# Kernel optimization log

Measured on AMD Instinct MI355X. Metric: run time of the kernel, lower is better.

Reference implementation:

```python
import jax, jax.numpy as jnp
import numpy as np

B, L, F, H = 8, 1024, 1024, 16
D = F // H  # feat_head = 64
EPS = 1e-5


def setup_inputs() -> dict:
    key = jax.random.key(0)
    ks = jax.random.split(key, 12)
    s = 1.0 / np.sqrt(F)
    inp = {
        "q": jax.random.normal(ks[0], (B, L, F), jnp.float32),
        "k": jax.random.normal(ks[1], (B, L, F), jnp.float32),
        "v": jax.random.normal(ks[2], (B, L, F), jnp.float32),
        "Wq": jax.random.uniform(ks[3], (F, F), jnp.float32, -s, s),
        "bq": jax.random.uniform(ks[4], (F,), jnp.float32, -s, s),
        "Wk": jax.random.uniform(ks[5], (F, F), jnp.float32, -s, s),
        "bk": jax.random.uniform(ks[6], (F,), jnp.float32, -s, s),
        "Wv": jax.random.uniform(ks[7], (F, F), jnp.float32, -s, s),
        "bv": jax.random.uniform(ks[8], (F,), jnp.float32, -s, s),
        "Wf": jax.random.uniform(ks[9], (F, F), jnp.float32, -s, s),
        "bf": jax.random.uniform(ks[10], (F,), jnp.float32, -s, s),
        "gamma": jnp.ones((F,), jnp.float32),
        "beta": jnp.zeros((F,), jnp.float32),
    }
    return inp


def _split_heads(x):
    # (B, L, F) -> (B*H, L, D), matching reshape->transpose(1,2)->reshape
    return x.reshape(B, L, H, D).transpose(0, 2, 1, 3).reshape(B * H, L, D)


def reference(q, k, v, Wq, bq, Wk, bk, Wv, bv, Wf, bf, gamma, beta):
    residual = q
    qh = _split_heads(q @ Wq.T + bq)
    kh = _split_heads(k @ Wk.T + bk)
    vh = _split_heads(v @ Wv.T + bv)
    # scores: (B*H, L, L)
    scores = jnp.einsum('nqd,nkd->nqk', qh, kh) / np.sqrt(D)
    raw_att = jax.nn.softmax(scores, axis=-1)
    att = jnp.einsum('nqk,nkd->nqd', raw_att, vh)  # (B*H, L, D)
    # faithful to original output recombine: reshape(H, B, L, D).permute(1,2,0,3)
    att = att.reshape(H, B, L, D).transpose(1, 2, 0, 3).reshape(B, L, F)
    att = att @ Wf.T + bf
    # dropout in eval mode = identity; activation is None
    x = att + residual
    mu = jnp.mean(x, axis=-1, keepdims=True)
    var = jnp.mean(jnp.square(x - mu), axis=-1, keepdims=True)
    out = (x - mu) * jax.lax.rsqrt(var + EPS) * gamma + beta
    return out, raw_att
```

## Files before the change

### kernel.cpp

```cpp
#include <hip/hip_runtime.h>

#define BB 8
#define LL 1024
#define FF 1024
#define HH 16
#define DD 64
#define NBH 128

typedef __attribute__((ext_vector_type(8))) short bf16x8;
typedef __attribute__((ext_vector_type(4))) float f32x4;

#define GLD_LDS16(g, l)                                                        \
  __builtin_amdgcn_global_load_lds(                                            \
      (const __attribute__((address_space(1))) unsigned int*)(g),              \
      (__attribute__((address_space(3))) unsigned int*)(l), 16, 0, 0)

__device__ __forceinline__ unsigned short f2bf(float f) {
  unsigned int u = __float_as_uint(f);
  unsigned int r = u + 0x7fffu + ((u >> 16) & 1u);
  return (unsigned short)(r >> 16);
}

__global__ __launch_bounds__(256) void cvt3_kernel(const float* __restrict__ s0,
                                                   const float* __restrict__ s1,
                                                   const float* __restrict__ s2,
                                                   short* __restrict__ dst, int n4) {
  int z = blockIdx.y;
  const float* src = (z == 0) ? s0 : (z == 1) ? s1 : s2;
  int i = blockIdx.x * 256 + threadIdx.x;
  if (i >= n4) return;
  float4 v = ((const float4*)src)[i];
  short4 o;
  o.x = (short)f2bf(v.x); o.y = (short)f2bf(v.y);
  o.z = (short)f2bf(v.z); o.w = (short)f2bf(v.w);
  ((short4*)(dst + (size_t)z * n4 * 4))[i] = o;
}

__global__ __launch_bounds__(256) void cvt4_kernel(const float* __restrict__ s0,
                                                   const float* __restrict__ s1,
                                                   const float* __restrict__ s2,
                                                   const float* __restrict__ s3,
                                                   short* __restrict__ dst, int n4) {
  int z = blockIdx.y;
  const float* src = (z == 0) ? s0 : (z == 1) ? s1 : (z == 2) ? s2 : s3;
  int i = blockIdx.x * 256 + threadIdx.x;
  if (i >= n4) return;
  float4 v = ((const float4*)src)[i];
  short4 o;
  o.x = (short)f2bf(v.x); o.y = (short)f2bf(v.y);
  o.z = (short)f2bf(v.z); o.w = (short)f2bf(v.w);
  ((short4*)(dst + (size_t)z * n4 * 4))[i] = o;
}

__global__ __launch_bounds__(256) void proj_qkv(
    const short* __restrict__ Aall, const short* __restrict__ Wall,
    const float* __restrict__ bq, const float* __restrict__ bk,
    const float* __restrict__ bv, short* __restrict__ Dall) {
  const int o = blockIdx.x + (blockIdx.y << 6) + (blockIdx.z << 9);
  const int n = ((o & 7) * 192) + (o >> 3);
  const int z = n >> 9;
  const int r = n & 511;
  const int by = r & 7, bx = r >> 3;

  const short* A  = Aall + (size_t)z * (BB * LL * FF);
  const short* Bt = Wall + (size_t)z * (FF * FF);
  const float* bias = (z == 0) ? bq : (z == 1) ? bk : bv;
  short* dst = Dall + (size_t)z * ((size_t)NBH * LL * DD);
  const float scale = (z == 0) ? 0.125f : 1.0f;

  __shared__ __attribute__((aligned(16))) short As[128 * 64];
  __shared__ __attribute__((aligned(16))) short Bs[128 * 64];

  const int tid = threadIdx.x;
  const int lane = tid & 63, w = tid >> 6;
  const int wr = w >> 1, wc = w & 1;
  const int row16 = lane & 15, kg = lane >> 4;
  const int m0 = bx * 128, n0 = by * 128;

  const f32x4 z4 = {0.f, 0.f, 0.f, 0.f};
  f32x4 acc[4][4];
  for (int i = 0; i < 4; ++i)
    for (int j = 0; j < 4; ++j) acc[i][j] = z4;

  for (int k0 = 0; k0 < FF; k0 += 64) {
#pragma unroll
    for (int rr = 0; rr < 4; ++rr) {
      int e8 = tid + rr * 256;
      int row = e8 >> 3, cs = ((e8 & 7) ^ (row & 7)) * 8;
      GLD_LDS16(A + (size_t)(m0 + row) * FF + k0 + cs, As + e8 * 8);
      GLD_LDS16(Bt + (size_t)(n0 + row) * FF + k0 + cs, Bs + e8 * 8);
    }
    __syncthreads();
#pragma unroll
    for (int kk2 = 0; kk2 < 2; ++kk2) {
      bf16x8 af[4], bfr[4];
#pragma unroll
      for (int i = 0; i < 4; ++i) {
        int ra = wr * 64 + i * 16 + row16;
        int rb = wc * 64 + i * 16 + row16;
        af[i]  = *(const bf16x8*)(As + ra * 64 + ((((kk2 << 2) | kg) ^ (ra & 7)) << 3));
        bfr[i] = *(const bf16x8*)(Bs + rb * 64 + ((((kk2 << 2) | kg) ^ (rb & 7)) << 3));
      }
#pragma unroll
      for (int i = 0; i < 4; ++i)
#pragma unroll
        for (int j = 0; j < 4; ++j)
          acc[i][j] = __builtin_amdgcn_mfma_f32_16x16x32_bf16(af[i], bfr[j], acc[i][j], 0, 0, 0);
    }
    __syncthreads();
  }

#pragma unroll
  for (int i = 0; i < 4; ++i) {
#pragma unroll
    for (int j = 0; j < 4; ++j) {
      int ncol = n0 + wc * 64 + j * 16 + row16;
      float bn = bias[ncol];
      int h = ncol >> 6, d = ncol & 63;
#pragma unroll
      for (int rr = 0; rr < 4; ++rr) {
        int m = m0 + wr * 64 + i * 16 + kg * 4 + rr;
        int b = m >> 10, l = m & 1023;
        float val = (acc[i][j][rr] + bn) * scale;
        dst[(((size_t)(b * HH + h)) * LL + l) * DD + d] = (short)f2bf(val);
      }
    }
  }
}

__global__ __launch_bounds__(256) void vtrans(const short* __restrict__ Vh,
                                              short* __restrict__ Vt) {
  const int bh = blockIdx.y;
  const int l0 = blockIdx.x * 64;
  __shared__ short T[64][72];
  const int tid = threadIdx.x;
#pragma unroll
  for (int r = 0; r < 2; ++r) {
    int e = tid + r * 256;
    int row = e >> 3, c8 = (e & 7) * 8;
    *(uint4*)(&T[row][c8]) = *(const uint4*)(Vh + ((size_t)bh * LL + l0 + row) * DD + c8);
  }
  __syncthreads();
#pragma unroll
  for (int r = 0; r < 2; ++r) {
    int e = tid + r * 256;
    int d = e >> 3, l8 = (e & 7) * 8;
    short tmp[8];
#pragma unroll
    for (int j = 0; j < 8; ++j) tmp[j] = T[l8 + j][d];
    *(uint4*)(Vt + ((size_t)bh * DD + d) * LL + l0 + l8) = *(uint4*)tmp;
  }
}

__global__ __launch_bounds__(256) void attn_kernel(
    const short* __restrict__ Qh, const short* __restrict__ Kh,
    const short* __restrict__ Vt, float* __restrict__ Patt,
    short* __restrict__ attb) {
  const int o = blockIdx.x + (blockIdx.y << 4);
  const int n = ((o & 7) << 8) + (o >> 3);
  const int bh = n >> 4;
  const int q0 = (n & 15) * 64;
  const int tid = threadIdx.x;
  const int lane = tid & 63, w = tid >> 6;
  const int row16 = lane & 15, kg = lane >> 4;

  __shared__ __attribute__((aligned(16))) short Qs[64 * 64];
  __shared__ __attribute__((aligned(16))) short Ks[64 * 64];
  __shared__ __attribute__((aligned(16))) short Vts[64 * 64];
  __shared__ __attribute__((aligned(16))) short PsT[4][16 * 64];

#pragma unroll
  for (int r = 0; r < 2; ++r) {
    int e8 = tid + r * 256;
    int row = e8 >> 3, c8 = (e8 & 7) ^ (row & 7);
    GLD_LDS16(Qh + ((size_t)bh * LL + q0 + row) * DD + c8 * 8, Qs + e8 * 8);
  }
  __syncthreads();
  const int qrow = w * 16 + row16;
  bf16x8 aq0 = *(const bf16x8*)(Qs + qrow * 64 + ((kg ^ (qrow & 7)) << 3));
  bf16x8 aq1 = *(const bf16x8*)(Qs + qrow * 64 + (((kg + 4) ^ (qrow & 7)) << 3));

  const f32x4 z4 = {0.f, 0.f, 0.f, 0.f};
  float lsum = 0.f;

  for (int k0 = 0; k0 < LL; k0 += 64) {
#pragma unroll
    for (int r = 0; r < 2; ++r) {
      int e8 = tid + r * 256;
      int row = e8 >> 3, c8 = (e8 & 7) ^ (row & 7);
      GLD_LDS16(Kh + ((size_t)bh * LL + k0 + row) * DD + c8 * 8, Ks + e8 * 8);
    }
    __syncthreads();
    f32x4 s[4] = {z4, z4, z4, z4};
#pragma unroll
    for (int t = 0; t < 4; ++t) {
      int krow = t * 16 + row16;
      bf16x8 b0 = *(const bf16x8*)(Ks + krow * 64 + ((kg ^ (krow & 7)) << 3));
      bf16x8 b1 = *(const bf16x8*)(Ks + krow * 64 + (((kg + 4) ^ (krow & 7)) << 3));
      s[t] = __builtin_amdgcn_mfma_f32_16x16x32_bf16(b0, aq0, s[t], 0, 0, 0);
      s[t] = __builtin_amdgcn_mfma_f32_16x16x32_bf16(b1, aq1, s[t], 0, 0, 0);
    }
#pragma unroll
    for (int t = 0; t < 4; ++t)
#pragma unroll
      for (int r = 0; r < 4; ++r) lsum += __expf(s[t][r]);
    __syncthreads();
  }
  lsum += __shfl_xor(lsum, 16);
  lsum += __shfl_xor(lsum, 32);
  const float linv = 1.0f / lsum;

  f32x4 oT[4] = {z4, z4, z4, z4};

  for (int k0 = 0; k0 < LL; k0 += 64) {
#pragma unroll
    for (int r = 0; r < 2; ++r) {
      int e8 = tid + r * 256;
      int row = e8 >> 3, c8 = (e8 & 7) ^ (row & 7);
      GLD_LDS16(Kh + ((size_t)bh * LL + k0 + row) * DD + c8 * 8, Ks + e8 * 8);
      GLD_LDS16(Vt + ((size_t)bh * DD + row) * LL + k0 + c8 * 8, Vts + e8 * 8);
    }
    __syncthreads();
    f32x4 s[4] = {z4, z4, z4, z4};
#pragma unroll
    for (int t = 0; t < 4; ++t) {
      int krow = t * 16 + row16;
      bf16x8 b0 = *(const bf16x8*)(Ks + krow * 64 + ((kg ^ (krow & 7)) << 3));
      bf16x8 b1 = *(const bf16x8*)(Ks + krow * 64 + (((kg + 4) ^ (krow & 7)) << 3));
      s[t] = __builtin_amdgcn_mfma_f32_16x16x32_bf16(b0, aq0, s[t], 0, 0, 0);
      s[t] = __builtin_amdgcn_mfma_f32_16x16x32_bf16(b1, aq1, s[t], 0, 0, 0);
    }
    const int qq = q0 + w * 16 + row16;
#pragma unroll
    for (int t = 0; t < 4; ++t) {
      f32x4 pv;
#pragma unroll
      for (int r = 0; r < 4; ++r) pv[r] = __expf(s[t][r]) * linv;
      __builtin_nontemporal_store(
          pv, (f32x4*)(Patt + ((size_t)bh * LL + qq) * LL + k0 + t * 16 + kg * 4));
      short4 ps;
      ps.x = (short)f2bf(pv[0]); ps.y = (short)f2bf(pv[1]);
      ps.z = (short)f2bf(pv[2]); ps.w = (short)f2bf(pv[3]);
      int c = ((t * 2 + (kg >> 1)) ^ (row16 & 7));
      *(short4*)(&PsT[w][row16 * 64 + c * 8 + (kg & 1) * 4]) = ps;
    }
    bf16x8 pb0 = *(const bf16x8*)(&PsT[w][row16 * 64 + ((kg ^ (row16 & 7)) << 3)]);
    bf16x8 pb1 = *(const bf16x8*)(&PsT[w][row16 * 64 + (((4 + kg) ^ (row16 & 7)) << 3)]);
#pragma unroll
    for (int td = 0; td < 4; ++td) {
      int trow = td * 16 + row16;
      bf16x8 v0 = *(const bf16x8*)(Vts + trow * 64 + ((kg ^ (trow & 7)) << 3));
      bf16x8 v1 = *(const bf16x8*)(Vts + trow * 64 + (((kg + 4) ^ (trow & 7)) << 3));
      oT[td] = __builtin_amdgcn_mfma_f32_16x16x32_bf16(v0, pb0, oT[td], 0, 0, 0);
      oT[td] = __builtin_amdgcn_mfma_f32_16x16x32_bf16(v1, pb1, oT[td], 0, 0, 0);
    }
    __syncthreads();
  }

  const int iblk = bh >> 3;
  const int jb = bh & 7;
  const int qq = q0 + w * 16 + row16;
#pragma unroll
  for (int td = 0; td < 4; ++td) {
    short4 ov;
    ov.x = (short)f2bf(oT[td][0]); ov.y = (short)f2bf(oT[td][1]);
    ov.z = (short)f2bf(oT[td][2]); ov.w = (short)f2bf(oT[td][3]);
    *(short4*)(attb + ((size_t)jb * LL + qq) * FF + iblk * 64 + td * 16 + kg * 4) = ov;
  }
}

__global__ __launch_bounds__(256) void proj_out(
    const short* __restrict__ A, const short* __restrict__ Bt,
    const float* __restrict__ bias, const float* __restrict__ resid,
    float* __restrict__ xb) {
  const int o = blockIdx.x + (blockIdx.y << 6);
  const int n = ((o & 7) << 6) + (o >> 3);
  const int by = n & 7, bx = n >> 3;

  __shared__ __attribute__((aligned(16))) short As[128 * 64];
  __shared__ __attribute__((aligned(16))) short Bs[128 * 64];

  const int tid = threadIdx.x;
  const int lane = tid & 63, w = tid >> 6;
  const int wr = w >> 1, wc = w & 1;
  const int row16 = lane & 15, kg = lane >> 4;
  const int m0 = bx * 128, n0 = by * 128;

  const f32x4 z4 = {0.f, 0.f, 0.f, 0.f};
  f32x4 acc[4][4];
  for (int i = 0; i < 4; ++i)
    for (int j = 0; j < 4; ++j) acc[i][j] = z4;

  for (int k0 = 0; k0 < FF; k0 += 64) {
#pragma unroll
    for (int rr = 0; rr < 4; ++rr) {
      int e8 = tid + rr * 256;
      int row = e8 >> 3, cs = ((e8 & 7) ^ (row & 7)) * 8;
      GLD_LDS16(A + (size_t)(m0 + row) * FF + k0 + cs, As + e8 * 8);
      GLD_LDS16(Bt + (size_t)(n0 + row) * FF + k0 + cs, Bs + e8 * 8);
    }
    __syncthreads();
#pragma unroll
    for (int kk2 = 0; kk2 < 2; ++kk2) {
      bf16x8 af[4], bfr[4];
#pragma unroll
      for (int i = 0; i < 4; ++i) {
        int ra = wr * 64 + i * 16 + row16;
        int rb = wc * 64 + i * 16 + row16;
        af[i]  = *(const bf16x8*)(As + ra * 64 + ((((kk2 << 2) | kg) ^ (ra & 7)) << 3));
        bfr[i] = *(const bf16x8*)(Bs + rb * 64 + ((((kk2 << 2) | kg) ^ (rb & 7)) << 3));
      }
#pragma unroll
      for (int i = 0; i < 4; ++i)
#pragma unroll
        for (int j = 0; j < 4; ++j)
          acc[i][j] = __builtin_amdgcn_mfma_f32_16x16x32_bf16(af[i], bfr[j], acc[i][j], 0, 0, 0);
    }
    __syncthreads();
  }

#pragma unroll
  for (int i = 0; i < 4; ++i) {
#pragma unroll
    for (int j = 0; j < 4; ++j) {
      int ncol = n0 + wc * 64 + j * 16 + row16;
      float bn = bias[ncol];
#pragma unroll
      for (int rr = 0; rr < 4; ++rr) {
        int m = m0 + wr * 64 + i * 16 + kg * 4 + rr;
        xb[(size_t)m * FF + ncol] = acc[i][j][rr] + bn + resid[(size_t)m * FF + ncol];
      }
    }
  }
}

__global__ __launch_bounds__(256) void ln_kernel(const float* __restrict__ xb,
                                                 const float* __restrict__ gamma,
                                                 const float* __restrict__ beta,
                                                 float* __restrict__ out) {
  const int row = blockIdx.x;
  const int tid = threadIdx.x;
  const float4 v = *(const float4*)(xb + (size_t)row * FF + tid * 4);
  float s = v.x + v.y + v.z + v.w;
  float s2 = v.x * v.x + v.y * v.y + v.z * v.z + v.w * v.w;
#pragma unroll
  for (int o = 1; o < 64; o <<= 1) {
    s += __shfl_xor(s, o);
    s2 += __shfl_xor(s2, o);
  }
  __shared__ float ss[4], ss2[4];
  int w = tid >> 6, lane = tid & 63;
  if (lane == 0) { ss[w] = s; ss2[w] = s2; }
  __syncthreads();
  s = ss[0] + ss[1] + ss[2] + ss[3];
  s2 = ss2[0] + ss2[1] + ss2[2] + ss2[3];
  float mu = s * (1.0f / 1024.0f);
  float var = s2 * (1.0f / 1024.0f) - mu * mu;
  float rs = rsqrtf(var + 1e-5f);
  float4 g = *(const float4*)(gamma + tid * 4);
  float4 be = *(const float4*)(beta + tid * 4);
  float4 o;
  o.x = (v.x - mu) * rs * g.x + be.x;
  o.y = (v.y - mu) * rs * g.y + be.y;
  o.z = (v.z - mu) * rs * g.z + be.z;
  o.w = (v.w - mu) * rs * g.w + be.w;
  *(float4*)(out + (size_t)row * FF + tid * 4) = o;
}

extern "C" void kernel_launch(void* const* d_in, const int* in_sizes, int n_in,
                              void* d_out, int out_size, void* d_ws, size_t ws_size,
                              hipStream_t stream) {
  const float* q  = (const float*)d_in[0];
  const float* k  = (const float*)d_in[1];
  const float* v  = (const float*)d_in[2];
  const float* Wq = (const float*)d_in[3];
  const float* bq = (const float*)d_in[4];
  const float* Wk = (const float*)d_in[5];
  const float* bk = (const float*)d_in[6];
  const float* Wv = (const float*)d_in[7];
  const float* bv = (const float*)d_in[8];
  const float* Wf = (const float*)d_in[9];
  const float* bf = (const float*)d_in[10];
  const float* gamma = (const float*)d_in[11];
  const float* beta  = (const float*)d_in[12];

  float* out = (float*)d_out;
  float* Patt = out + (size_t)BB * LL * FF;

  char* ws = (char*)d_ws;
  const size_t MB = (size_t)1 << 20;
  short* qb = (short*)(ws + 0 * MB);
  short* Wb = (short*)(ws + 48 * MB);
  short* Qh = (short*)(ws + 56 * MB);
  short* Kh = (short*)(ws + 72 * MB);
  short* Vh = (short*)(ws + 88 * MB);
  short* attb = qb;
  short* Vt = (short*)(ws + 16 * MB);
  float* xb = (float*)(ws + 16 * MB);

  const int nAct4 = BB * LL * FF / 4;
  const int nW4 = FF * FF / 4;
  cvt3_kernel<<<dim3((nAct4 + 255) / 256, 3), 256, 0, stream>>>(q, k, v, qb, nAct4);
  cvt4_kernel<<<dim3((nW4 + 255) / 256, 4), 256, 0, stream>>>(Wq, Wk, Wv, Wf, Wb, nW4);

  proj_qkv<<<dim3(64, 8, 3), 256, 0, stream>>>(qb, Wb, bq, bk, bv, Qh);
  vtrans<<<dim3(16, 128), 256, 0, stream>>>(Vh, Vt);
  attn_kernel<<<dim3(16, 128), 256, 0, stream>>>(Qh, Kh, Vt, Patt, attb);
  proj_out<<<dim3(64, 8), 256, 0, stream>>>(attb, Wb + 3 * (size_t)FF * FF, bf, q, xb);
  ln_kernel<<<8192, 256, 0, stream>>>(xb, gamma, beta, out);
}
```

Baseline: 324.8 us.

## Fuse V transpose into QKV projection epilogue, double-buffer attention K/V tiles, use exp2

The QKV projection now stages its output tile in LDS and writes it back with coalesced 16-byte stores. For V it writes the tile transposed, which removes the separate vtrans kernel and its extra round trip through memory. The attention kernel double-buffers the K and V tiles so global-to-LDS loads overlap with MFMA work. It also folds log2(e) into the Q scale so softmax can use exp2 with a log-sum subtraction instead of exp followed by a multiply. The LDS footprint of proj_qkv grows and the attention kernel uses more shared memory, which may reduce occupancy.

```diff
diff --git a/kernel.cpp b/kernel.cpp
--- a/kernel.cpp
+++ b/kernel.cpp
@@ -66,10 +66,11 @@
   const short* Bt = Wall + (size_t)z * (FF * FF);
   const float* bias = (z == 0) ? bq : (z == 1) ? bk : bv;
   short* dst = Dall + (size_t)z * ((size_t)NBH * LL * DD);
-  const float scale = (z == 0) ? 0.125f : 1.0f;
-
-  __shared__ __attribute__((aligned(16))) short As[128 * 64];
-  __shared__ __attribute__((aligned(16))) short Bs[128 * 64];
+  const float scale = (z == 0) ? 0.125f * 1.44269504088896f : 1.0f;
+
+  __shared__ __attribute__((aligned(16))) short LB[128 * 136];
+  short* As = LB;
+  short* Bs = LB + 128 * 64;
 
   const int tid = threadIdx.x;
   const int lane = tid & 63, w = tid >> 6;
@@ -110,45 +111,39 @@
     __syncthreads();
   }
 
+  const int z2 = (z == 2);
 #pragma unroll
   for (int i = 0; i < 4; ++i) {
 #pragma unroll
     for (int j = 0; j < 4; ++j) {
-      int ncol = n0 + wc * 64 + j * 16 + row16;
-      float bn = bias[ncol];
-      int h = ncol >> 6, d = ncol & 63;
+      int nl = wc * 64 + j * 16 + row16;
+      float bn = bias[n0 + nl];
 #pragma unroll
       for (int rr = 0; rr < 4; ++rr) {
-        int m = m0 + wr * 64 + i * 16 + kg * 4 + rr;
-        int b = m >> 10, l = m & 1023;
+        int ml = wr * 64 + i * 16 + kg * 4 + rr;
         float val = (acc[i][j][rr] + bn) * scale;
-        dst[(((size_t)(b * HH + h)) * LL + l) * DD + d] = (short)f2bf(val);
+        int rrow = z2 ? nl : ml, ccol = z2 ? ml : nl;
+        LB[rrow * 136 + ccol] = (short)f2bf(val);
       }
     }
   }
-}
-
-__global__ __launch_bounds__(256) void vtrans(const short* __restrict__ Vh,
-                                              short* __restrict__ Vt) {
-  const int bh = blockIdx.y;
-  const int l0 = blockIdx.x * 64;
-  __shared__ short T[64][72];
-  const int tid = threadIdx.x;
-#pragma unroll
-  for (int r = 0; r < 2; ++r) {
-    int e = tid + r * 256;
-    int row = e >> 3, c8 = (e & 7) * 8;
-    *(uint4*)(&T[row][c8]) = *(const uint4*)(Vh + ((size_t)bh * LL + l0 + row) * DD + c8);
-  }
   __syncthreads();
-#pragma unroll
-  for (int r = 0; r < 2; ++r) {
-    int e = tid + r * 256;
-    int d = e >> 3, l8 = (e & 7) * 8;
-    short tmp[8];
-#pragma unroll
-    for (int j = 0; j < 8; ++j) tmp[j] = T[l8 + j][d];
-    *(uint4*)(Vt + ((size_t)bh * DD + d) * LL + l0 + l8) = *(uint4*)tmp;
+  const int b = m0 >> 10;
+  const int lbase = m0 & 1023;
+#pragma unroll
+  for (int rr = 0; rr < 8; ++rr) {
+    int e = tid + rr * 256;
+    int row = e >> 4, c8 = e & 15;
+    uint4 val = *(const uint4*)(LB + row * 136 + c8 * 8);
+    if (!z2) {
+      int l = lbase + row;
+      int h = (n0 + c8 * 8) >> 6, d = (c8 & 7) * 8;
+      *(uint4*)(dst + (((size_t)(b * HH + h)) * LL + l) * DD + d) = val;
+    } else {
+      int h = (n0 + row) >> 6, d = (n0 + row) & 63;
+      int l = lbase + c8 * 8;
+      *(uint4*)(dst + (((size_t)(b * HH + h)) * DD + d) * LL + l) = val;
+    }
   }
 }
 
@@ -165,16 +160,36 @@
   const int row16 = lane & 15, kg = lane >> 4;
 
   __shared__ __attribute__((aligned(16))) short Qs[64 * 64];
-  __shared__ __attribute__((aligned(16))) short Ks[64 * 64];
-  __shared__ __attribute__((aligned(16))) short Vts[64 * 64];
+  __shared__ __attribute__((aligned(16))) short Ks[2][64 * 64];
+  __shared__ __attribute__((aligned(16))) short Vts[2][64 * 64];
   __shared__ __attribute__((aligned(16))) short PsT[4][16 * 64];
 
-#pragma unroll
-  for (int r = 0; r < 2; ++r) {
-    int e8 = tid + r * 256;
-    int row = e8 >> 3, c8 = (e8 & 7) ^ (row & 7);
-    GLD_LDS16(Qh + ((size_t)bh * LL + q0 + row) * DD + c8 * 8, Qs + e8 * 8);
-  }
+#define STAGE_K(tt, bb)                                                        \
+  {                                                                            \
+    int e8a = tid, rowa = e8a >> 3, c8a = (e8a & 7) ^ (rowa & 7);              \
+    GLD_LDS16(Kh + ((size_t)bh * LL + (tt) * 64 + rowa) * DD + c8a * 8,        \
+              &Ks[bb][e8a * 8]);                                               \
+    int e8b = tid + 256, rowb = e8b >> 3, c8b = (e8b & 7) ^ (rowb & 7);        \
+    GLD_LDS16(Kh + ((size_t)bh * LL + (tt) * 64 + rowb) * DD + c8b * 8,        \
+              &Ks[bb][e8b * 8]);                                               \
+  }
+#define STAGE_V(tt, bb)                                                        \
+  {                                                                            \
+    int e8a = tid, rowa = e8a >> 3, c8a = (e8a & 7) ^ (rowa & 7);              \
+    GLD_LDS16(Vt + ((size_t)bh * DD + rowa) * LL + (tt) * 64 + c8a * 8,        \
+              &Vts[bb][e8a * 8]);                                              \
+    int e8b = tid + 256, rowb = e8b >> 3, c8b = (e8b & 7) ^ (rowb & 7);        \
+    GLD_LDS16(Vt + ((size_t)bh * DD + rowb) * LL + (tt) * 64 + c8b * 8,        \
+              &Vts[bb][e8b * 8]);                                              \
+  }
+
+  {
+    int e8a = tid, rowa = e8a >> 3, c8a = (e8a & 7) ^ (rowa & 7);
+    GLD_LDS16(Qh + ((size_t)bh * LL + q0 + rowa) * DD + c8a * 8, Qs + e8a * 8);
+    int e8b = tid + 256, rowb = e8b >> 3, c8b = (e8b & 7) ^ (rowb & 7);
+    GLD_LDS16(Qh + ((size_t)bh * LL + q0 + rowb) * DD + c8b * 8, Qs + e8b * 8);
+  }
+  STAGE_K(0, 0);
   __syncthreads();
   const int qrow = w * 16 + row16;
   bf16x8 aq0 = *(const bf16x8*)(Qs + qrow * 64 + ((kg ^ (qrow & 7)) << 3));
@@ -183,65 +198,61 @@
   const f32x4 z4 = {0.f, 0.f, 0.f, 0.f};
   float lsum = 0.f;
 
-  for (int k0 = 0; k0 < LL; k0 += 64) {
-#pragma unroll
-    for (int r = 0; r < 2; ++r) {
-      int e8 = tid + r * 256;
-      int row = e8 >> 3, c8 = (e8 & 7) ^ (row & 7);
-      GLD_LDS16(Kh + ((size_t)bh * LL + k0 + row) * DD + c8 * 8, Ks + e8 * 8);
-    }
-    __syncthreads();
+  for (int t = 0; t < 16; ++t) {
+    int cur = t & 1;
+    if (t < 15) STAGE_K(t + 1, cur ^ 1);
     f32x4 s[4] = {z4, z4, z4, z4};
 #pragma unroll
-    for (int t = 0; t < 4; ++t) {
-      int krow = t * 16 + row16;
-      bf16x8 b0 = *(const bf16x8*)(Ks + krow * 64 + ((kg ^ (krow & 7)) << 3));
-      bf16x8 b1 = *(const bf16x8*)(Ks + krow * 64 + (((kg + 4) ^ (krow & 7)) << 3));
-      s[t] = __builtin_amdgcn_mfma_f32_16x16x32_bf16(b0, aq0, s[t], 0, 0, 0);
-      s[t] = __builtin_amdgcn_mfma_f32_16x16x32_bf16(b1, aq1, s[t], 0, 0, 0);
-    }
-#pragma unroll
-    for (int t = 0; t < 4; ++t)
-#pragma unroll
-      for (int r = 0; r < 4; ++r) lsum += __expf(s[t][r]);
+    for (int tt = 0; tt < 4; ++tt) {
+      int krow = tt * 16 + row16;
+      bf16x8 b0 = *(const bf16x8*)(&Ks[cur][krow * 64 + ((kg ^ (krow & 7)) << 3)]);
+      bf16x8 b1 = *(const bf16x8*)(&Ks[cur][krow * 64 + (((kg + 4) ^ (krow & 7)) << 3)]);
+      s[tt] = __builtin_amdgcn_mfma_f32_16x16x32_bf16(b0, aq0, s[tt], 0, 0, 0);
+      s[tt] = __builtin_amdgcn_mfma_f32_16x16x32_bf16(b1, aq1, s[tt], 0, 0, 0);
+    }
+#pragma unroll
+    for (int tt = 0; tt < 4; ++tt)
+#pragma unroll
+      for (int rr = 0; rr < 4; ++rr) lsum += exp2f(s[tt][rr]);
     __syncthreads();
   }
   lsum += __shfl_xor(lsum, 16);
   lsum += __shfl_xor(lsum, 32);
-  const float linv = 1.0f / lsum;
+  const float lc = __log2f(lsum);
 
   f32x4 oT[4] = {z4, z4, z4, z4};
 
-  for (int k0 = 0; k0 < LL; k0 += 64) {
-#pragma unroll
-    for (int r = 0; r < 2; ++r) {
-      int e8 = tid + r * 256;
-      int row = e8 >> 3, c8 = (e8 & 7) ^ (row & 7);
-      GLD_LDS16(Kh + ((size_t)bh * LL + k0 + row) * DD + c8 * 8, Ks + e8 * 8);
-      GLD_LDS16(Vt + ((size_t)bh * DD + row) * LL + k0 + c8 * 8, Vts + e8 * 8);
-    }
-    __syncthreads();
+  STAGE_K(0, 0);
+  STAGE_V(0, 0);
+  __syncthreads();
+  for (int t = 0; t < 16; ++t) {
+    int cur = t & 1;
+    if (t < 15) {
+      STAGE_K(t + 1, cur ^ 1);
+      STAGE_V(t + 1, cur ^ 1);
+    }
     f32x4 s[4] = {z4, z4, z4, z4};
 #pragma unroll
-    for (int t = 0; t < 4; ++t) {
-      int krow = t * 16 + row16;
-      bf16x8 b0 = *(const bf16x8*)(Ks + krow * 64 + ((kg ^ (krow & 7)) << 3));
-      bf16x8 b1 = *(const bf16x8*)(Ks + krow * 64 + (((kg + 4) ^ (krow & 7)) << 3));
-      s[t] = __builtin_amdgcn_mfma_f32_16x16x32_bf16(b0, aq0, s[t], 0, 0, 0);
-      s[t] = __builtin_amdgcn_mfma_f32_16x16x32_bf16(b1, aq1, s[t], 0, 0, 0);
+    for (int tt = 0; tt < 4; ++tt) {
+      int krow = tt * 16 + row16;
+      bf16x8 b0 = *(const bf16x8*)(&Ks[cur][krow * 64 + ((kg ^ (krow & 7)) << 3)]);
+      bf16x8 b1 = *(const bf16x8*)(&Ks[cur][krow * 64 + (((kg + 4) ^ (krow & 7)) << 3)]);
+      s[tt] = __builtin_amdgcn_mfma_f32_16x16x32_bf16(b0, aq0, s[tt], 0, 0, 0);
+      s[tt] = __builtin_amdgcn_mfma_f32_16x16x32_bf16(b1, aq1, s[tt], 0, 0, 0);
     }
     const int qq = q0 + w * 16 + row16;
-#pragma unroll
-    for (int t = 0; t < 4; ++t) {
+    const int k0 = t * 64;
+#pragma unroll
+    for (int tt = 0; tt < 4; ++tt) {
       f32x4 pv;
 #pragma unroll
-      for (int r = 0; r < 4; ++r) pv[r] = __expf(s[t][r]) * linv;
+      for (int rr = 0; rr < 4; ++rr) pv[rr] = exp2f(s[tt][rr] - lc);
       __builtin_nontemporal_store(
-          pv, (f32x4*)(Patt + ((size_t)bh * LL + qq) * LL + k0 + t * 16 + kg * 4));
+          pv, (f32x4*)(Patt + ((size_t)bh * LL + qq) * LL + k0 + tt * 16 + kg * 4));
       short4 ps;
       ps.x = (short)f2bf(pv[0]); ps.y = (short)f2bf(pv[1]);
       ps.z = (short)f2bf(pv[2]); ps.w = (short)f2bf(pv[3]);
-      int c = ((t * 2 + (kg >> 1)) ^ (row16 & 7));
+      int c = ((tt * 2 + (kg >> 1)) ^ (row16 & 7));
       *(short4*)(&PsT[w][row16 * 64 + c * 8 + (kg & 1) * 4]) = ps;
     }
     bf16x8 pb0 = *(const bf16x8*)(&PsT[w][row16 * 64 + ((kg ^ (row16 & 7)) << 3)]);
@@ -249,8 +260,8 @@
 #pragma unroll
     for (int td = 0; td < 4; ++td) {
       int trow = td * 16 + row16;
-      bf16x8 v0 = *(const bf16x8*)(Vts + trow * 64 + ((kg ^ (trow & 7)) << 3));
-      bf16x8 v1 = *(const bf16x8*)(Vts + trow * 64 + (((kg + 4) ^ (trow & 7)) << 3));
+      bf16x8 v0 = *(const bf16x8*)(&Vts[cur][trow * 64 + ((kg ^ (trow & 7)) << 3)]);
+      bf16x8 v1 = *(const bf16x8*)(&Vts[cur][trow * 64 + (((kg + 4) ^ (trow & 7)) << 3)]);
       oT[td] = __builtin_amdgcn_mfma_f32_16x16x32_bf16(v0, pb0, oT[td], 0, 0, 0);
       oT[td] = __builtin_amdgcn_mfma_f32_16x16x32_bf16(v1, pb1, oT[td], 0, 0, 0);
     }
@@ -267,6 +278,8 @@
     ov.z = (short)f2bf(oT[td][2]); ov.w = (short)f2bf(oT[td][3]);
     *(short4*)(attb + ((size_t)jb * LL + qq) * FF + iblk * 64 + td * 16 + kg * 4) = ov;
   }
+#undef STAGE_K
+#undef STAGE_V
 }
 
 __global__ __launch_bounds__(256) void proj_out(
@@ -393,9 +406,8 @@
   short* Wb = (short*)(ws + 48 * MB);
   short* Qh = (short*)(ws + 56 * MB);
   short* Kh = (short*)(ws + 72 * MB);
-  short* Vh = (short*)(ws + 88 * MB);
+  short* Vt = (short*)(ws + 88 * MB);
   short* attb = qb;
-  short* Vt = (short*)(ws + 16 * MB);
   float* xb = (float*)(ws + 16 * MB);
 
   const int nAct4 = BB * LL * FF / 4;
@@ -404,7 +416,6 @@
   cvt4_kernel<<<dim3((nW4 + 255) / 256, 4), 256, 0, stream>>>(Wq, Wk, Wv, Wf, Wb, nW4);
 
   proj_qkv<<<dim3(64, 8, 3), 256, 0, stream>>>(qb, Wb, bq, bk, bv, Qh);
-  vtrans<<<dim3(16, 128), 256, 0, stream>>>(Vh, Vt);
   attn_kernel<<<dim3(16, 128), 256, 0, stream>>>(Qh, Kh, Vt, Patt, attb);
   proj_out<<<dim3(64, 8), 256, 0, stream>>>(attb, Wb + 3 * (size_t)FF * FF, bf, q, xb);
   ln_kernel<<<8192, 256, 0, stream>>>(xb, gamma, beta, out);
```

After: 303.5 us. 1.07x faster.
